# Performance work log

Measured on AMD Instinct MI355X. Metric: run time of the kernel, lower is better.

Reference implementation:

```python
import jax, jax.numpy as jnp
import numpy as np

EMBED_DIM = 1024
NUM_HEADS = 16
HEAD_DIM = EMBED_DIM // NUM_HEADS


def setup_inputs() -> dict:
    key = jax.random.key(0)
    k_x, k_wqkv, k_bqkv, k_wo, k_bo = jax.random.split(key, 5)
    B, T, C = 4, 2048, EMBED_DIM
    # PyTorch Linear default init scale ~ 1/sqrt(fan_in); use small normals
    s = 1.0 / np.sqrt(C)
    return {
        "x": jax.random.normal(k_x, (B, T, C), dtype=jnp.float32),
        "w_qkv": jax.random.normal(k_wqkv, (C, 3 * C), dtype=jnp.float32) * s,
        "b_qkv": jax.random.normal(k_bqkv, (3 * C,), dtype=jnp.float32) * s,
        "w_out": jax.random.normal(k_wo, (C, C), dtype=jnp.float32) * s,
        "b_out": jax.random.normal(k_bo, (C,), dtype=jnp.float32) * s,
    }


def reference(x, w_qkv, b_qkv, w_out, b_out):
    B, T, C = x.shape
    H, D = NUM_HEADS, HEAD_DIM
    qkv = x @ w_qkv + b_qkv                      # (B, T, 3C)
    q, k, v = jnp.split(qkv, 3, axis=-1)
    # (B, H, T, D)
    q = q.reshape(B, T, H, D).transpose(0, 2, 1, 3)
    k = k.reshape(B, T, H, D).transpose(0, 2, 1, 3)
    v = v.reshape(B, T, H, D).transpose(0, 2, 1, 3)
    scores = jnp.einsum("bhqd,bhkd->bhqk", q, k) / jnp.sqrt(jnp.float32(D))
    causal = jnp.tril(jnp.ones((T, T), dtype=bool))  # (T, T)
    scores = jnp.where(causal[None, None, :, :], scores, -jnp.inf)
    attn = jax.nn.softmax(scores, axis=-1)
    out = jnp.einsum("bhqk,bhkd->bhqd", attn, v)  # (B, H, T, D)
    out = out.transpose(0, 2, 1, 3).reshape(B, T, C)
    return out @ w_out + b_out
```

## Files before the change

### kernel.cpp

```cpp
#include <hip/hip_runtime.h>
#include <hip/hip_bf16.h>

#define B_  4
#define T_  2048
#define C_  1024
#define H_  16
#define D_  64
#define BH_ (B_*H_)

typedef float  f32x4  __attribute__((ext_vector_type(4)));
typedef __bf16 bf16x8 __attribute__((ext_vector_type(8)));
typedef __bf16 bf16x2 __attribute__((ext_vector_type(2)));

static __device__ __forceinline__ ushort f2bf(float f) {
    union { float f; unsigned u; } x; x.f = f;
    unsigned r = ((x.u >> 16) & 1u) + 0x7fffu;
    return (ushort)((x.u + r) >> 16);
}

static __device__ __forceinline__ uint packbf(float a, float b) {
    bf16x2 v = { (__bf16)a, (__bf16)b };
    return __builtin_bit_cast(uint, v);
}

static __device__ __forceinline__ void gload_lds16(const void* g, void* l) {
    __builtin_amdgcn_global_load_lds(
        (const __attribute__((address_space(1))) unsigned int*)g,
        (__attribute__((address_space(3))) unsigned int*)l, 16, 0, 0);
}

template<int N> static __device__ __forceinline__ void waitcnt_vm() {
    if constexpr (N == 0) asm volatile("s_waitcnt vmcnt(0)" ::: "memory");
    else if constexpr (N == 3) asm volatile("s_waitcnt vmcnt(3)" ::: "memory");
    else if constexpr (N == 4) asm volatile("s_waitcnt vmcnt(4)" ::: "memory");
    else static_assert(N == 0 || N == 3 || N == 4);
    __builtin_amdgcn_sched_barrier(0);
}
static __device__ __forceinline__ void lgkm0() {
    asm volatile("s_waitcnt lgkmcnt(0)" ::: "memory");
    __builtin_amdgcn_sched_barrier(0);
}

__global__ void cvt_kernel(const float* __restrict__ in, ushort* __restrict__ out, int n) {
    int i = (blockIdx.x * blockDim.x + threadIdx.x) * 4;
    if (i < n) {
        float4 v = *(const float4*)(in + i);
        ushort4 o;
        o.x = f2bf(v.x); o.y = f2bf(v.y); o.z = f2bf(v.z); o.w = f2bf(v.w);
        *(ushort4*)(out + i) = o;
    }
}

__global__ void transpose_cvt_kernel(const float* __restrict__ in, ushort* __restrict__ out,
                                     int K, int N) {
    __shared__ float tile[32][33];
    int k0 = blockIdx.y * 32, n0 = blockIdx.x * 32;
    int tx = threadIdx.x & 31, ty = threadIdx.x >> 5;
    #pragma unroll
    for (int r = 0; r < 32; r += 8)
        tile[ty + r][tx] = in[(size_t)(k0 + ty + r) * N + n0 + tx];
    __syncthreads();
    #pragma unroll
    for (int r = 0; r < 32; r += 8)
        out[(size_t)(n0 + ty + r) * K + k0 + tx] = f2bf(tile[tx][ty + r]);
}

template<int NFR, bool QKV>
__global__ __launch_bounds__(512, 2) void gemm_hk(
    const ushort* __restrict__ A,
    const ushort* __restrict__ Bt,
    const float*  __restrict__ bias,
    void* __restrict__ outp,
    ushort* __restrict__ vtp)
{
    constexpr int NT   = 16;
    constexpr int BN   = NFR * 64;
    constexpr int ABUF = 32768;
    constexpr int BBUF = BN * 128;
    constexpr int LB   = (NFR == 4) ? 2 : 1;
    constexpr int PK   = 2 + LB;
    __shared__ __align__(16) char lds[2 * ABUF + 2 * BBUF];
    char* ldsB = lds + 2 * ABUF;

    const int gX   = gridDim.x;
    const int orig = blockIdx.y * gX + blockIdx.x;
    const int cpx  = (gX * gridDim.y) >> 3;
    const int wg   = (orig & 7) * cpx + (orig >> 3);
    const int m0 = (wg / gX) * 256, n0 = (wg % gX) * BN;

    const int tid = threadIdx.x, lane = tid & 63;
    const int wv = tid >> 6, wm = wv >> 2, wn = wv & 3;
    const int lr = lane & 15, lh = lane >> 4;

    const int sc = (tid & 3) ^ ((tid >> 2) & 3);
    const ushort* aA = A  + (size_t)(m0 + (tid >> 2)) * 1024 + sc * 8;
    const ushort* aB = Bt + (size_t)(n0 + (tid >> 2)) * 1024 + sc * 8;

    const int cxor = (lh ^ (lr & 3)) * 16;
    const int arow = (wm * 128 + lr) * 64 + cxor;
    const int brow = (wn * (NFR * 16) + lr) * 64 + cxor;

    f32x4 acc[8][NFR] = {};

    auto stage_a = [&](int buf, int t, int kh) {
        #pragma unroll
        for (int p = 0; p < 2; ++p)
            gload_lds16(aA + (size_t)p * 131072 + t * 64 + kh * 32,
                        lds + buf * ABUF + kh * 16384 + p * 8192 + tid * 16);
    };
    auto stage_b = [&](int buf, int t, int kh) {
        #pragma unroll
        for (int p = 0; p < LB; ++p)
            gload_lds16(aB + (size_t)p * 131072 + t * 64 + kh * 32,
                        ldsB + buf * BBUF + kh * (BBUF / 2) + p * 8192 + tid * 16);
    };
    auto read_a = [&](bf16x8 (&af)[8], int buf, int kh) {
        const char* base = lds + buf * ABUF + kh * 16384 + arow;
        #pragma unroll
        for (int mi = 0; mi < 8; ++mi) af[mi] = *(const bf16x8*)(base + mi * 1024);
    };
    auto read_b = [&](bf16x8& b0, bf16x8& b1, int buf, int kh, int nh) {
        const char* base = ldsB + buf * BBUF + kh * (BBUF / 2) + brow + nh * 2048;
        b0 = *(const bf16x8*)(base);
        b1 = *(const bf16x8*)(base + 1024);
    };

#define MFMA2(NI, BB0, BB1)                                                          \
    do {                                                                             \
        __builtin_amdgcn_s_setprio(1);                                               \
        _Pragma("unroll")                                                            \
        for (int mi = 0; mi < 8; ++mi) {                                             \
            acc[mi][NI]     = __builtin_amdgcn_mfma_f32_16x16x32_bf16(af[mi], BB0,   \
                                                     acc[mi][NI], 0, 0, 0);          \
            acc[mi][NI + 1] = __builtin_amdgcn_mfma_f32_16x16x32_bf16(af[mi], BB1,   \
                                                     acc[mi][NI + 1], 0, 0, 0);      \
        }                                                                            \
        __builtin_amdgcn_s_setprio(0);                                               \
    } while (0)

    stage_a(0, 0, 0); stage_b(0, 0, 0);
    stage_a(0, 0, 1); stage_b(0, 0, 1);
    waitcnt_vm<PK>();
    __builtin_amdgcn_s_barrier();

    for (int t = 0; t < NT; ++t) {
        const int cur = t & 1, nxt = cur ^ 1;
        const bool pf = (t + 1 < NT);
        bf16x8 af[8], b0, b1;
        if constexpr (NFR == 4) {
            read_a(af, cur, 0); read_b(b0, b1, cur, 0, 0);
            if (pf) stage_a(nxt, t + 1, 0);
            __builtin_amdgcn_s_barrier();
            lgkm0();
            MFMA2(0, b0, b1);
            read_b(b0, b1, cur, 0, 1);
            if (pf) stage_b(nxt, t + 1, 0);
            if (t < NT - 1) waitcnt_vm<4>(); else waitcnt_vm<0>();
            __builtin_amdgcn_s_barrier();
            lgkm0();
            MFMA2(2, b0, b1);
            read_a(af, cur, 1); read_b(b0, b1, cur, 1, 0);
            if (pf) stage_a(nxt, t + 1, 1);
            __builtin_amdgcn_s_barrier();
            lgkm0();
            MFMA2(0, b0, b1);
            read_b(b0, b1, cur, 1, 1);
            if (pf) stage_b(nxt, t + 1, 1);
            if (t < NT - 1) waitcnt_vm<4>();
            __builtin_amdgcn_s_barrier();
            lgkm0();
            MFMA2(2, b0, b1);
        } else {
            read_a(af, cur, 0); read_b(b0, b1, cur, 0, 0);
            if (pf) { stage_a(nxt, t + 1, 0); stage_b(nxt, t + 1, 0); }
            if (t < NT - 1) waitcnt_vm<3>(); else waitcnt_vm<0>();
            __builtin_amdgcn_s_barrier();
            lgkm0();
            MFMA2(0, b0, b1);
            read_a(af, cur, 1); read_b(b0, b1, cur, 1, 0);
            if (pf) { stage_a(nxt, t + 1, 1); stage_b(nxt, t + 1, 1); }
            if (t < NT - 1) waitcnt_vm<3>();
            __builtin_amdgcn_s_barrier();
            lgkm0();
            MFMA2(0, b0, b1);
        }
    }
#undef MFMA2

    #pragma unroll
    for (int mi = 0; mi < 8; ++mi) {
        #pragma unroll
        for (int ni = 0; ni < NFR; ++ni) {
            int col = n0 + wn * (NFR * 16) + ni * 16 + lr;
            float bv = bias[col];
            if constexpr (QKV) {
                ushort* qkv = (ushort*)outp;
                int which = col >> 10;
                int h = (col & 1023) >> 6;
                int d = col & 63;
                if (which == 2) {
                    #pragma unroll
                    for (int r = 0; r < 4; ++r) {
                        int row = m0 + wm * 128 + mi * 16 + lh * 4 + r;
                        int b = row >> 11, tt = row & 2047;
                        vtp[(((size_t)(b * H_ + h)) * D_ + d) * T_ + tt] =
                            f2bf(acc[mi][ni][r] + bv);
                    }
                } else {
                    #pragma unroll
                    for (int r = 0; r < 4; ++r) {
                        int row = m0 + wm * 128 + mi * 16 + lh * 4 + r;
                        int b = row >> 11, tt = row & 2047;
                        float v = acc[mi][ni][r] + bv;
                        if (which == 0) v *= 0.18033688011112042f;
                        qkv[(size_t)which * (BH_ * T_ * D_) +
                            (((size_t)(b * H_ + h)) * T_ + tt) * D_ + d] = f2bf(v);
                    }
                }
            } else {
                float* Cout = (float*)outp;
                #pragma unroll
                for (int r = 0; r < 4; ++r) {
                    int row = m0 + wm * 128 + mi * 16 + lh * 4 + r;
                    Cout[(size_t)row * C_ + col] = acc[mi][ni][r] + bv;
                }
            }
        }
    }
}

__global__ __launch_bounds__(256, 4) void flash_kernel(
    const ushort* __restrict__ qb,
    const ushort* __restrict__ kb,
    const ushort* __restrict__ vt,
    ushort* __restrict__ ob)
{
    __shared__ __align__(16) ushort sK[2][64 * 64];
    __shared__ __align__(16) ushort sV[2][64 * 64];
    __shared__ __align__(16) ushort sP[4][16 * 64];
    const int wg  = ((blockIdx.x & 7) << 7) | (blockIdx.x >> 3);
    const int bh  = wg >> 4;
    const int pr  = wg & 15;
    const int qtA = pr, qtB = 31 - pr;
    const int lane = threadIdx.x & 63, wv = threadIdx.x >> 6;
    const int lr = lane & 15, lh = lane >> 4;

    const ushort* qrowA = qb + ((size_t)bh * T_ + qtA * 64 + wv * 16 + lr) * D_;
    const ushort* qrowB = qb + ((size_t)bh * T_ + qtB * 64 + wv * 16 + lr) * D_;
    bf16x8 qfA0 = *(const bf16x8*)(qrowA + lh * 8);
    bf16x8 qfA1 = *(const bf16x8*)(qrowA + 32 + lh * 8);
    bf16x8 qfB0 = *(const bf16x8*)(qrowB + lh * 8);
    bf16x8 qfB1 = *(const bf16x8*)(qrowB + 32 + lh * 8);

    const int srow = lane >> 3;
    const int scol = ((lane & 7) ^ srow) * 8;
    const ushort* kbase = kb + (size_t)bh * T_ * D_;
    const ushort* vbase = vt + (size_t)bh * D_ * T_;

    const int sw   = (lr & 7) << 4;
    const int off0 = (16 * lh) ^ sw;
    const int off1 = (64 + 16 * lh) ^ sw;

    f32x4 oA[4] = {}, oB[4] = {};
    float mA = -1e30f, lA = 0.f, mB = -1e30f, lB = 0.f;

    auto redmax = [&](float x) {
        x = fmaxf(x, __int_as_float(__builtin_amdgcn_ds_swizzle(__float_as_int(x), 0x401F)));
        x = fmaxf(x, __shfl_xor(x, 32, 64));
        return x;
    };
    auto redsum = [&](float x) {
        x += __int_as_float(__builtin_amdgcn_ds_swizzle(__float_as_int(x), 0x401F));
        x += __shfl_xor(x, 32, 64);
        return x;
    };

    auto tile = [&](f32x4 (&o)[4], float& mrow, float& lsum,
                    const bf16x8& q0f, const bf16x8& q1f,
                    const char* K0, const char* V0, bool diag) {
        f32x4 s[4];
        __builtin_amdgcn_s_setprio(1);
        #pragma unroll
        for (int nt = 0; nt < 4; ++nt) {
            const char* krow = K0 + (nt * 16 + lr) * 128;
            bf16x8 k0 = *(const bf16x8*)(krow + off0);
            bf16x8 k1 = *(const bf16x8*)(krow + off1);
            f32x4 a = {0.f, 0.f, 0.f, 0.f};
            a = __builtin_amdgcn_mfma_f32_16x16x32_bf16(k0, q0f, a, 0, 0, 0);
            a = __builtin_amdgcn_mfma_f32_16x16x32_bf16(k1, q1f, a, 0, 0, 0);
            s[nt] = a;
        }
        __builtin_amdgcn_s_setprio(0);
        if (diag) {
            #pragma unroll
            for (int nt = 0; nt < 4; ++nt)
                #pragma unroll
                for (int r = 0; r < 4; ++r)
                    if (nt * 16 + lh * 4 + r > wv * 16 + lr) s[nt][r] = -INFINITY;
        }

        float pmax = fmaxf(fmaxf(fmaxf(s[0][0], s[0][1]), fmaxf(s[0][2], s[0][3])),
                           fmaxf(fmaxf(s[1][0], s[1][1]), fmaxf(s[1][2], s[1][3])));
        pmax = fmaxf(pmax, fmaxf(fmaxf(fmaxf(s[2][0], s[2][1]), fmaxf(s[2][2], s[2][3])),
                                 fmaxf(fmaxf(s[3][0], s[3][1]), fmaxf(s[3][2], s[3][3]))));
        pmax = redmax(pmax);

        if (__any(pmax > mrow + 8.f)) {
            float mnew = fmaxf(mrow, pmax);
            float al = __builtin_exp2f(mrow - mnew);
            lsum *= al;
            #pragma unroll
            for (int r = 0; r < 4; ++r) {
                float ar = __shfl(al, lh * 20 + r, 64);
                o[0][r] *= ar; o[1][r] *= ar; o[2][r] *= ar; o[3][r] *= ar;
            }
            mrow = mnew;
        }

        float rsum = 0.f;
        uint pk[8];
        #pragma unroll
        for (int nt = 0; nt < 4; ++nt) {
            float p0 = __builtin_exp2f(s[nt][0] - mrow);
            float p1 = __builtin_exp2f(s[nt][1] - mrow);
            float p2 = __builtin_exp2f(s[nt][2] - mrow);
            float p3 = __builtin_exp2f(s[nt][3] - mrow);
            rsum += (p0 + p1) + (p2 + p3);
            pk[nt * 2]     = packbf(p0, p1);
            pk[nt * 2 + 1] = packbf(p2, p3);
        }
        lsum += redsum(rsum);

        char* P = (char*)sP[wv];
        {
            char* prow = P + lr * 128;
            #pragma unroll
            for (int nt = 0; nt < 4; ++nt) {
                uint2 w; w.x = pk[nt * 2]; w.y = pk[nt * 2 + 1];
                *(uint2*)(prow + ((32 * nt + 8 * lh) ^ sw)) = w;
            }
        }
        asm volatile("" ::: "memory");
        bf16x8 pf0 = *(const bf16x8*)(P + lr * 128 + off0);
        bf16x8 pf1 = *(const bf16x8*)(P + lr * 128 + off1);

        __builtin_amdgcn_s_setprio(1);
        #pragma unroll
        for (int dt = 0; dt < 4; ++dt) {
            const char* vrow = V0 + (dt * 16 + lr) * 128;
            bf16x8 v0 = *(const bf16x8*)(vrow + off0);
            bf16x8 v1 = *(const bf16x8*)(vrow + off1);
            o[dt] = __builtin_amdgcn_mfma_f32_16x16x32_bf16(pf0, v0, o[dt], 0, 0, 0);
            o[dt] = __builtin_amdgcn_mfma_f32_16x16x32_bf16(pf1, v1, o[dt], 0, 0, 0);
        }
        __builtin_amdgcn_s_setprio(0);
    };

    #pragma unroll
    for (int i = 0; i < 2; ++i) {
        int j = i * 4 + wv;
        gload_lds16(kbase + (size_t)(j * 8 + srow) * D_ + scol, &sK[0][j * 512]);
        gload_lds16(vbase + (size_t)(j * 8 + srow) * T_ + scol, &sV[0][j * 512]);
    }
    __syncthreads();

    for (int kt = 0; kt <= qtB; ++kt) {
        const int cur = kt & 1;
        if (kt < qtB) {
            const int nb = cur ^ 1;
            #pragma unroll
            for (int i = 0; i < 2; ++i) {
                int j = i * 4 + wv;
                gload_lds16(kbase + (size_t)((kt + 1) * 64 + j * 8 + srow) * D_ + scol, &sK[nb][j * 512]);
                gload_lds16(vbase + (size_t)(j * 8 + srow) * T_ + (kt + 1) * 64 + scol, &sV[nb][j * 512]);
            }
        }
        const char* K0 = (const char*)sK[cur];
        const char* V0 = (const char*)sV[cur];
        if (kt <= qtA) tile(oA, mA, lA, qfA0, qfA1, K0, V0, kt == qtA);
        tile(oB, mB, lB, qfB0, qfB1, K0, V0, kt == qtB);
        __syncthreads();
    }

    const int b = bh >> 4, h = bh & 15;
    auto writeout = [&](f32x4 (&o)[4], float lsum, int q0) {
        float inv = 1.f / lsum;
        #pragma unroll
        for (int r = 0; r < 4; ++r) {
            float ir = __shfl(inv, lh * 20 + r, 64);
            int q = q0 + lh * 4 + r;
            #pragma unroll
            for (int dt = 0; dt < 4; ++dt)
                ob[((size_t)b * T_ + q) * C_ + h * 64 + dt * 16 + lr] = f2bf(o[dt][r] * ir);
        }
    };
    writeout(oA, lA, qtA * 64 + wv * 16);
    writeout(oB, lB, qtB * 64 + wv * 16);
}

extern "C" void kernel_launch(void* const* d_in, const int* in_sizes, int n_in,
                              void* d_out, int out_size, void* d_ws, size_t ws_size,
                              hipStream_t stream) {
    const float* x     = (const float*)d_in[0];
    const float* w_qkv = (const float*)d_in[1];
    const float* b_qkv = (const float*)d_in[2];
    const float* w_out = (const float*)d_in[3];
    const float* b_out = (const float*)d_in[4];
    float* out = (float*)d_out;

    char* ws = (char*)d_ws;
    ushort* xb     = (ushort*)(ws + 0);
    ushort* wqkvT  = (ushort*)(ws + 16777216);
    ushort* woutT  = (ushort*)(ws + 23068672);
    ushort* qkv    = (ushort*)(ws + 25165824);
    ushort* vT     = (ushort*)(ws + 75497472);
    ushort* attn   = xb;
    ushort* qb = qkv;
    ushort* kb = qkv + (size_t)BH_ * T_ * D_;

    const int nx = B_ * T_ * C_;
    cvt_kernel<<<nx / 4 / 256, 256, 0, stream>>>(x, xb, nx);
    transpose_cvt_kernel<<<dim3(3 * C_ / 32, C_ / 32), 256, 0, stream>>>(w_qkv, wqkvT, C_, 3 * C_);
    transpose_cvt_kernel<<<dim3(C_ / 32, C_ / 32), 256, 0, stream>>>(w_out, woutT, C_, C_);
    gemm_hk<4, true><<<dim3(3 * C_ / 256, B_ * T_ / 256), 512, 0, stream>>>(xb, wqkvT, b_qkv, qkv, vT);
    flash_kernel<<<BH_ * 16, 256, 0, stream>>>(qb, kb, vT, attn);
    gemm_hk<2, false><<<dim3(C_ / 128, B_ * T_ / 256), 512, 0, stream>>>(attn, woutT, b_out, out, nullptr);
}
```

Baseline: 210.9 us.

## Permute K row mapping so P stays in registers, dropping LDS round-trip

The K rows fed to the QK^T MFMA are permuted so that each lane's softmax probabilities already sit in the register layout the PV MFMA expects as its A operand. The per-wave shared-memory P buffer, its writes and its reads are removed. The causal mask index is updated to match the permuted key order. This cuts LDS traffic and latency in the inner loop and lowers LDS usage. The cost is a more complex K address computation and a correctness dependence on the permutation matching the MFMA operand layout.

```diff
diff --git a/kernel.cpp b/kernel.cpp
--- a/kernel.cpp
+++ b/kernel.cpp
@@ -237,7 +237,6 @@
 {
     __shared__ __align__(16) ushort sK[2][64 * 64];
     __shared__ __align__(16) ushort sV[2][64 * 64];
-    __shared__ __align__(16) ushort sP[4][16 * 64];
     const int wg  = ((blockIdx.x & 7) << 7) | (blockIdx.x >> 3);
     const int bh  = wg >> 4;
     const int pr  = wg & 15;
@@ -257,9 +256,9 @@
     const ushort* kbase = kb + (size_t)bh * T_ * D_;
     const ushort* vbase = vt + (size_t)bh * D_ * T_;
 
-    const int sw   = (lr & 7) << 4;
-    const int off0 = (16 * lh) ^ sw;
-    const int off1 = (64 + 16 * lh) ^ sw;
+    const int swv  = (lr & 7) << 4;
+    const int off0 = (16 * lh) ^ swv;
+    const int off1 = (64 + 16 * lh) ^ swv;
 
     f32x4 oA[4] = {}, oB[4] = {};
     float mA = -1e30f, lA = 0.f, mB = -1e30f, lB = 0.f;
@@ -282,9 +281,11 @@
         __builtin_amdgcn_s_setprio(1);
         #pragma unroll
         for (int nt = 0; nt < 4; ++nt) {
-            const char* krow = K0 + (nt * 16 + lr) * 128;
-            bf16x8 k0 = *(const bf16x8*)(krow + off0);
-            bf16x8 k1 = *(const bf16x8*)(krow + off1);
+            const int kk  = ((lr >> 2) << 3) | (lr & 3) | ((nt & 1) << 2) | ((nt >> 1) << 5);
+            const int swk = (kk & 7) << 4;
+            const char* krow = K0 + kk * 128;
+            bf16x8 k0 = *(const bf16x8*)(krow + ((16 * lh) ^ swk));
+            bf16x8 k1 = *(const bf16x8*)(krow + ((64 + 16 * lh) ^ swk));
             f32x4 a = {0.f, 0.f, 0.f, 0.f};
             a = __builtin_amdgcn_mfma_f32_16x16x32_bf16(k0, q0f, a, 0, 0, 0);
             a = __builtin_amdgcn_mfma_f32_16x16x32_bf16(k1, q1f, a, 0, 0, 0);
@@ -293,10 +294,12 @@
         __builtin_amdgcn_s_setprio(0);
         if (diag) {
             #pragma unroll
-            for (int nt = 0; nt < 4; ++nt)
+            for (int nt = 0; nt < 4; ++nt) {
+                const int kb0 = 8 * lh + 4 * (nt & 1) + 32 * (nt >> 1);
                 #pragma unroll
                 for (int r = 0; r < 4; ++r)
-                    if (nt * 16 + lh * 4 + r > wv * 16 + lr) s[nt][r] = -INFINITY;
+                    if (kb0 + r > wv * 16 + lr) s[nt][r] = -INFINITY;
+            }
         }
 
         float pmax = fmaxf(fmaxf(fmaxf(s[0][0], s[0][1]), fmaxf(s[0][2], s[0][3])),
@@ -331,18 +334,10 @@
         }
         lsum += redsum(rsum);
 
-        char* P = (char*)sP[wv];
-        {
-            char* prow = P + lr * 128;
-            #pragma unroll
-            for (int nt = 0; nt < 4; ++nt) {
-                uint2 w; w.x = pk[nt * 2]; w.y = pk[nt * 2 + 1];
-                *(uint2*)(prow + ((32 * nt + 8 * lh) ^ sw)) = w;
-            }
-        }
-        asm volatile("" ::: "memory");
-        bf16x8 pf0 = *(const bf16x8*)(P + lr * 128 + off0);
-        bf16x8 pf1 = *(const bf16x8*)(P + lr * 128 + off1);
+        uint4 w0 = {pk[0], pk[1], pk[2], pk[3]};
+        uint4 w1 = {pk[4], pk[5], pk[6], pk[7]};
+        bf16x8 pf0 = __builtin_bit_cast(bf16x8, w0);
+        bf16x8 pf1 = __builtin_bit_cast(bf16x8, w1);
 
         __builtin_amdgcn_s_setprio(1);
         #pragma unroll
```

After: 203.9 us. -3.3%, faster.
